# Performance work log

Measured on AMD Instinct MI355X. Metric: run time of the kernel, lower is better.

Reference implementation:

```python
import jax, jax.numpy as jnp
import numpy as np
import math

B, C, H, WIN = 8, 96, 224, 7
D_STATE, DT_RANK = 16, 6
PERK = C // 4
K_RATIO = 0.25


def nearest_perfect_square(val):
    if val <= 0:
        return 0
    s = math.sqrt(val)
    lo = math.floor(s) ** 2
    hi = math.ceil(s) ** 2
    return lo if abs(lo - val) <= abs(hi - val) else hi


def setup_inputs() -> dict:
    key = jax.random.key(0)
    ks = jax.random.split(key, 8)
    x = jax.random.normal(ks[0], (B, C, H, H), dtype=jnp.float32)
    router_w1 = jax.random.normal(ks[1], (C // 4, C), jnp.float32) * (1.0 / math.sqrt(C))
    router_b1 = jnp.zeros((C // 4,), jnp.float32)
    router_w2 = jax.random.normal(ks[2], (1, C // 4), jnp.float32) * (1.0 / math.sqrt(C // 4))
    router_b2 = jnp.zeros((1,), jnp.float32)
    x_proj_weight = jax.random.normal(ks[3], (4, DT_RANK + 2 * D_STATE, PERK), jnp.float32) * (1.0 / math.sqrt(PERK))
    std = DT_RANK ** -0.5
    dt_projs_weight = jax.random.uniform(ks[4], (4, PERK, DT_RANK), jnp.float32, -std, std)
    dt = jnp.exp(jax.random.uniform(ks[5], (4, PERK), jnp.float32) * (math.log(0.1) - math.log(0.001)) + math.log(0.001))
    dt = jnp.clip(dt, 1e-4)
    dt_projs_bias = dt + jnp.log(-jnp.expm1(-dt))  # inv-softplus init as in dt_init_fn
    A_logs = jnp.log(jnp.tile(jnp.arange(1, D_STATE + 1, dtype=jnp.float32)[None, :], (4 * PERK, 1)))
    Ds = jnp.ones((4 * PERK,), jnp.float32)
    return {"x": x, "router_w1": router_w1, "router_b1": router_b1, "router_w2": router_w2,
            "router_b2": router_b2, "x_proj_weight": x_proj_weight, "dt_projs_weight": dt_projs_weight,
            "dt_projs_bias": dt_projs_bias, "A_logs": A_logs, "Ds": Ds}


def reference(x, router_w1, router_b1, router_w2, router_b2, x_proj_weight,
              dt_projs_weight, dt_projs_bias, A_logs, Ds):
    Bb, Cc, Hh, Ww = x.shape
    nH = Hh // WIN
    N = nH * nH
    # window partition: b c (nh p1) (nw p2) -> b (nh nw) c p1 p2
    windows = x.reshape(Bb, Cc, nH, WIN, nH, WIN).transpose(0, 2, 4, 1, 3, 5).reshape(Bb, N, Cc, WIN, WIN)
    # router scores
    pooled = windows.mean(axis=(-2, -1))  # [B,N,C]
    hid = jax.nn.gelu(pooled @ router_w1.T + router_b1, approximate=False)
    logits = (hid @ router_w2.T + router_b2)[..., 0]  # [B,N]
    probs = jax.nn.softmax(logits, axis=1)
    top_k = min(max(nearest_perfect_square(N * K_RATIO), 1), N)
    n = int(math.isqrt(top_k))
    rw, sel = jax.lax.top_k(probs, top_k)  # sorted descending, like torch.topk
    windows_flat = windows.reshape(Bb, N, -1)
    cur = jnp.take_along_axis(windows_flat, sel[:, :, None], axis=1)  # [B,topk,C*w*w]
    cur = cur.reshape(Bb, n, n, Cc, WIN, WIN)
    L = n * n * WIN * WIN
    # channel interleave (p k) -> (k p), k=4
    x_int = cur.reshape(Bb, n, n, Cc // 4, 4, WIN, WIN).transpose(0, 1, 2, 4, 3, 5, 6)  # [B,n,n,4,perK,w,w]

    def local_scan(w, column_first, flip):
        # w: [B,n,n,D,wh,ww] -> [B,D,L]
        if column_first:
            w = w.transpose(0, 3, 2, 1, 5, 4)
        else:
            w = w.transpose(0, 3, 1, 2, 4, 5)
        w = w.reshape(Bb, -1, L)
        if flip:
            w = w[..., ::-1]
        return w

    xs = jnp.stack([
        local_scan(x_int[:, :, :, 0], False, False),
        local_scan(x_int[:, :, :, 1], True, False),
        local_scan(x_int[:, :, :, 2], False, True),
        local_scan(x_int[:, :, :, 3], True, True),
    ], axis=1)  # [B,4,perK,L]

    x_dbl = jnp.einsum('bkdl,kcd->bkcl', xs, x_proj_weight)
    dts = x_dbl[:, :, :DT_RANK]
    Bmat = x_dbl[:, :, DT_RANK:DT_RANK + D_STATE]  # [B,4,Nst,L]
    Cmat = x_dbl[:, :, DT_RANK + D_STATE:]
    dts = jnp.einsum('bkrl,kdr->bkdl', dts, dt_projs_weight)  # [B,4,perK,L]
    A_g = -jnp.exp(A_logs).reshape(4, PERK, D_STATE)
    delta = jax.nn.softplus(dts + dt_projs_bias.reshape(4, PERK)[None, :, :, None])

    # selective scan (grouped): h_{l} = exp(delta*A)*h_{l-1} + delta*u*B_l ; y_l = <h_l, C_l>
    dl = jnp.moveaxis(delta, -1, 0)  # [L,B,4,perK]
    ul = jnp.moveaxis(xs, -1, 0)
    Bl = jnp.moveaxis(Bmat, -1, 0)   # [L,B,4,Nst]
    Cl = jnp.moveaxis(Cmat, -1, 0)
    h0 = jnp.zeros((Bb, 4, PERK, D_STATE), jnp.float32)

    def step(h, inp):
        d, u, Bt, Ct = inp
        h = jnp.exp(d[..., None] * A_g) * h + (d * u)[..., None] * Bt[:, :, None, :]
        return h, jnp.einsum('bkdn,bkn->bkd', h, Ct)

    _, ys = jax.lax.scan(step, h0, (dl, ul, Bl, Cl))
    y = jnp.moveaxis(ys, 0, -1) + xs * Ds.reshape(4, PERK)[None, :, :, None]  # [B,4,perK,L]

    def local_reverse(yk, column_first, flip):
        if flip:
            yk = yk[..., ::-1]
        if column_first:
            yk = yk.reshape(Bb, -1, n, n, WIN, WIN).transpose(0, 1, 3, 5, 2, 4).reshape(Bb, -1, L)
        else:
            yk = yk.reshape(Bb, -1, n, n, WIN, WIN).transpose(0, 1, 2, 4, 3, 5).reshape(Bb, -1, L)
        return yk

    yout = jnp.concatenate([
        local_reverse(y[:, 0], False, False),
        local_reverse(y[:, 1], True, False),
        local_reverse(y[:, 2], False, True),
        local_reverse(y[:, 3], True, True),
    ], axis=1)  # [B,C,L]
    yout = yout.reshape(Bb, Cc, n * n, WIN * WIN).transpose(0, 2, 1, 3).reshape(Bb, top_k, -1)
    cur_out = yout * rw[:, :, None]
    residual = windows_flat * probs[:, :, None]
    residual = residual.at[jnp.arange(Bb)[:, None], sel].set(cur_out)
    new = windows_flat + residual
    return new.reshape(Bb, Cc, -1)
```

## Files before the change

### kernel.cpp

```cpp
#include <hip/hip_runtime.h>
#include <math.h>

#define BBATCH 8
#define CC 96
#define HH 224
#define NHW 32
#define NWIN 1024
#define TOPK 256
#define PERK 24
#define DST 16
#define DTR 6
#define LL 12544
#define LCP 52
#define NG 13
#define TCH 256
#define NBK 32
#define XROW 1248
#define WST4 2080

#define OFF_POOL 0
#define OFF_LOG  786432
#define OFF_PROB 794624
#define OFF_RW   802816
#define OFF_RANK 804864
#define OFF_SEL  813056
#define OFF_WEFF 815104
#define OFF_CP   820480
#define OFF_CS   3966208
#define OFF_XSD  7111936
#define OFF_STG  17335552

#define ROR_ADD(v, CTRL) \
    v += __int_as_float(__builtin_amdgcn_update_dpp(0, __float_as_int(v), CTRL, 0xf, 0xf, true))

__device__ __forceinline__ unsigned f2b(float f) {
    unsigned u = __float_as_uint(f);
    return (u + 0x7fffu + ((u >> 16) & 1u)) >> 16;
}
__device__ __forceinline__ unsigned pk(float a, float b) {
    return f2b(a) | (f2b(b) << 16);
}
__device__ __forceinline__ float lo_f(unsigned w) { return __uint_as_float(w << 16); }
__device__ __forceinline__ float hi_f(unsigned w) { return __uint_as_float(w & 0xffff0000u); }

__global__ void k_pool(const float* __restrict__ x, float* __restrict__ pooled) {
    int bc = blockIdx.x;
    const float* xp = x + (size_t)bc * HH * HH;
    float* pp = pooled + (size_t)bc * NWIN;
    for (int w = threadIdx.x; w < NWIN; w += blockDim.x) {
        int wr = w >> 5, wc = w & 31;
        const float* base = xp + (wr * 7) * HH + wc * 7;
        float s = 0.f;
        #pragma unroll
        for (int i = 0; i < 7; ++i) {
            #pragma unroll
            for (int j = 0; j < 7; ++j) s += base[i * HH + j];
        }
        pp[w] = s * (1.0f / 49.0f);
    }
}

__global__ __launch_bounds__(64) void k_router(
        const float* __restrict__ pooled,
        const float* __restrict__ w1, const float* __restrict__ b1,
        const float* __restrict__ w2, const float* __restrict__ b2,
        const float* __restrict__ xpw, const float* __restrict__ dtw,
        float* __restrict__ wcomb, float* __restrict__ logits) {
    __shared__ float sw1[PERK * CC];
    __shared__ float sb1[PERK];
    __shared__ float sw2[PERK];
    int b = blockIdx.x >> 4, slice = blockIdx.x & 15;
    int tid = threadIdx.x;
    for (int i = blockIdx.x * 64 + tid; i < 4 * 56 * PERK; i += 128 * 64) {
        int k = i / (56 * PERK), rem = i - k * (56 * PERK);
        int row = rem / PERK, c = rem - row * PERK;
        float v;
        if (row < PERK) {
            v = 0.f;
            #pragma unroll
            for (int r = 0; r < DTR; ++r)
                v += dtw[(k * PERK + row) * DTR + r] * xpw[(k * 38 + r) * PERK + c];
        } else {
            v = xpw[(k * 38 + (row - PERK + DTR)) * PERK + c];
        }
        wcomb[i] = v;
    }
    for (int i = tid; i < PERK * CC; i += 64) sw1[i] = w1[i];
    if (tid < PERK) { sb1[tid] = b1[tid]; sw2[tid] = w2[tid]; }
    __syncthreads();
    int w = slice * 64 + tid;
    float hid[PERK];
    #pragma unroll
    for (int j = 0; j < PERK; ++j) hid[j] = sb1[j];
    const float* pp = pooled + (size_t)b * CC * NWIN + w;
    for (int c = 0; c < CC; ++c) {
        float pv = pp[(size_t)c * NWIN];
        #pragma unroll
        for (int j = 0; j < PERK; ++j) hid[j] += pv * sw1[j * CC + c];
    }
    float lg = b2[0];
    #pragma unroll
    for (int j = 0; j < PERK; ++j) {
        float hv = hid[j];
        float g = 0.5f * hv * (1.0f + erff(hv * 0.7071067811865476f));
        lg += g * sw2[j];
    }
    logits[b * NWIN + w] = lg;
}

__global__ __launch_bounds__(64) void k_rankF(const float* __restrict__ logits,
        float* __restrict__ probs, float* __restrict__ rw,
        int* __restrict__ rank, int* __restrict__ sel) {
    __shared__ __attribute__((aligned(16))) float sp[NWIN];
    __shared__ float red[64];
    int b = blockIdx.x >> 4, slice = blockIdx.x & 15;
    int tid = threadIdx.x;
    for (int i = tid; i < NWIN / 4; i += 64)
        ((float4*)sp)[i] = ((const float4*)(logits + (size_t)b * NWIN))[i];
    __syncthreads();
    float m = -1e30f;
    for (int i = tid; i < NWIN; i += 64) m = fmaxf(m, sp[i]);
    red[tid] = m; __syncthreads();
    for (int o = 32; o > 0; o >>= 1) { if (tid < o) red[tid] = fmaxf(red[tid], red[tid + o]); __syncthreads(); }
    float mx = red[0]; __syncthreads();
    for (int i = tid; i < NWIN; i += 64) sp[i] = expf(sp[i] - mx);
    __syncthreads();
    float s = 0.f;
    for (int i = tid; i < NWIN; i += 64) s += sp[i];
    red[tid] = s; __syncthreads();
    for (int o = 32; o > 0; o >>= 1) { if (tid < o) red[tid] += red[tid + o]; __syncthreads(); }
    float sum = red[0]; __syncthreads();
    for (int i = tid; i < NWIN; i += 64) sp[i] = sp[i] / sum;
    __syncthreads();
    int w = slice * 64 + tid;
    float p = sp[w];
    probs[b * NWIN + w] = p;
    int r = 0;
    for (int j = 0; j < NWIN; j += 4) {
        float4 pj = *(const float4*)&sp[j];
        r += (int)((pj.x > p) || (pj.x == p && (j + 0) < w));
        r += (int)((pj.y > p) || (pj.y == p && (j + 1) < w));
        r += (int)((pj.z > p) || (pj.z == p && (j + 2) < w));
        r += (int)((pj.w > p) || (pj.w == p && (j + 3) < w));
    }
    rank[b * NWIN + w] = r;
    if (r < TOPK) { sel[b * TOPK + r] = w; rw[b * TOPK + r] = p; }
}

__device__ __forceinline__ float softplus_f(float v) {
    return fmaxf(v, 0.f) + __logf(1.0f + __expf(-fabsf(v)));
}

__device__ __forceinline__ int window_wsel(const int* sel, int b, int k, int t) {
    int qscan = (k >= 2) ? (255 - t) : t;
    int selidx = (k & 1) ? (((qscan & 15) << 4) | (qscan >> 4)) : qscan;
    return sel[b * TOPK + selidx];
}

__global__ __launch_bounds__(256) void k_gather(const float* __restrict__ x,
        const int* __restrict__ sel, float* __restrict__ xsd) {
    const int total = NBK * TCH * XROW;
    for (int e = blockIdx.x * 256 + threadIdx.x; e < total; e += gridDim.x * 256) {
        int blk = e / XROW;
        int rem = e - blk * XROW;
        int d2 = rem / LCP, j = rem - d2 * LCP;
        float v = 0.f;
        if (j < 49) {
            int t = blk & 255, bk = blk >> 8, k = bk & 3, b = bk >> 2;
            int wsel = window_wsel(sel, b, k, t);
            int pix = (k >= 2) ? 48 - j : j;
            int q7 = pix / 7, r7 = pix - q7 * 7;
            int wi = (k & 1) ? r7 : q7;
            int wj = (k & 1) ? q7 : r7;
            v = x[(((size_t)b * CC + 4 * d2 + k) * HH + (wsel >> 5) * 7 + wi) * HH
                  + (wsel & 31) * 7 + wj];
        }
        xsd[e] = v;
    }
}

__global__ __launch_bounds__(384, 4) void k_prodT(
        const float* __restrict__ xsd, const float* __restrict__ wcomb,
        const float* __restrict__ dtb, const float* __restrict__ alogs,
        float* __restrict__ stage, float* __restrict__ carrP, float* __restrict__ carrS) {
    __shared__ __attribute__((aligned(16))) float sxs[PERK][LCP];
    __shared__ __attribute__((aligned(16))) float sprj[56][LCP];
    __shared__ float swt[56 * PERK];
    __shared__ float sbias[PERK];
    int blk = blockIdx.x; int k = (blk >> 8) & 3;
    int tid = threadIdx.x;
    const float4* xin = (const float4*)(xsd + (size_t)blk * XROW);
    for (int i = tid; i < XROW / 4; i += 384) ((float4*)sxs)[i] = xin[i];
    for (int i = tid; i < 56 * PERK; i += 384) swt[i] = wcomb[k * (56 * PERK) + i];
    if (tid < PERK) sbias[tid] = dtb[k * PERK + tid];
    if (tid < 168) { int r = tid / 3, j = 49 + tid % 3; sprj[r][j] = 0.f; }
    __syncthreads();
    if (tid < 28 * NG) {
        int rp = tid / NG, g = tid - rp * NG; int j = g * 4;
        int row0 = rp * 2, row1 = row0 + 1;
        bool isdl = (row0 < PERK);
        float bs0 = isdl ? sbias[row0] : 0.f;
        float bs1 = isdl ? sbias[row1] : 0.f;
        float a0x = bs0, a0y = bs0, a0z = bs0, a0w = bs0;
        float a1x = bs1, a1y = bs1, a1z = bs1, a1w = bs1;
        #pragma unroll
        for (int d2 = 0; d2 < PERK; ++d2) {
            float w0 = swt[row0 * PERK + d2];
            float w1 = swt[row1 * PERK + d2];
            float4 v = *(const float4*)&sxs[d2][j];
            a0x += w0 * v.x; a0y += w0 * v.y; a0z += w0 * v.z; a0w += w0 * v.w;
            a1x += w1 * v.x; a1y += w1 * v.y; a1z += w1 * v.z; a1w += w1 * v.w;
        }
        if (isdl) {
            a0x = softplus_f(a0x); a0y = softplus_f(a0y); a0z = softplus_f(a0z); a0w = softplus_f(a0w);
            a1x = softplus_f(a1x); a1y = softplus_f(a1y); a1z = softplus_f(a1z); a1w = softplus_f(a1w);
        }
        if (g < 12) {
            float4 o0 = {a0x, a0y, a0z, a0w}; *(float4*)&sprj[row0][j] = o0;
            float4 o1 = {a1x, a1y, a1z, a1w}; *(float4*)&sprj[row1][j] = o1;
        } else {
            sprj[row0][j] = a0x; sprj[row1][j] = a1x;
        }
    }
    __syncthreads();
    uint4* sgP = (uint4*)(stage + (size_t)blk * WST4);
    uint4* sgQ = sgP + 312;
    for (int tsk = tid; tsk < 312; tsk += 384) {
        int g4 = tsk / 24, d2 = tsk - g4 * 24; int j = g4 * 4;
        uint4 o;
        o.x = pk(sprj[d2][j + 0], sxs[d2][j + 0]);
        o.y = pk(sprj[d2][j + 1], sxs[d2][j + 1]);
        o.z = pk(sprj[d2][j + 2], sxs[d2][j + 2]);
        o.w = pk(sprj[d2][j + 3], sxs[d2][j + 3]);
        sgP[tsk] = o;
    }
    for (int tsk = tid; tsk < 208; tsk += 384) {
        int g4 = tsk / 16, s2 = tsk - g4 * 16; int j = g4 * 4;
        uint4 o;
        o.x = pk(sprj[24 + s2][j + 0], sprj[40 + s2][j + 0]);
        o.y = pk(sprj[24 + s2][j + 1], sprj[40 + s2][j + 1]);
        o.z = pk(sprj[24 + s2][j + 2], sprj[40 + s2][j + 2]);
        o.w = pk(sprj[24 + s2][j + 3], sprj[40 + s2][j + 3]);
        sgQ[tsk] = o;
    }
    int d = tid >> 4, s = tid & 15;
    float A = -__expf(alogs[(k * PERK + d) * DST + s]);
    float P = 1.f, S = 0.f;
    for (int g = 0; g < NG; ++g) {
        int j = g * 4;
        float4 dl4 = *(const float4*)&sprj[d][j];
        float4 xs4 = *(const float4*)&sxs[d][j];
        float4 B4  = *(const float4*)&sprj[24 + s][j];
        float aa;
        aa = __expf(dl4.x * A); S = aa * S + (dl4.x * xs4.x) * B4.x; P *= aa;
        aa = __expf(dl4.y * A); S = aa * S + (dl4.y * xs4.y) * B4.y; P *= aa;
        aa = __expf(dl4.z * A); S = aa * S + (dl4.z * xs4.z) * B4.z; P *= aa;
        aa = __expf(dl4.w * A); S = aa * S + (dl4.w * xs4.w) * B4.w; P *= aa;
    }
    size_t cidx = (size_t)blk * 384 + tid;
    carrP[cidx] = P; carrS[cidx] = S;
}

__global__ void k_carry(const float* carrP, const float* carrS, float* hin) {
    int gid = blockIdx.x * blockDim.x + threadIdx.x;
    int bk = gid / 384, ds = gid - bk * 384;
    float Hv = 0.f;
    for (int t = 0; t < TCH; ++t) {
        size_t idx = ((size_t)bk * TCH + t) * 384 + ds;
        float pv = carrP[idx], sv = carrS[idx];
        hin[idx] = Hv;
        Hv = pv * Hv + sv;
    }
}

__global__ __launch_bounds__(64) void k_base(const float* __restrict__ x,
        const float* __restrict__ probs, const int* __restrict__ rank,
        float* __restrict__ out) {
    int wr = blockIdx.x % NHW; int bc = blockIdx.x / NHW;
    int b = bc / CC;
    __shared__ float buf[7 * HH];
    __shared__ float fmul[NHW];
    __shared__ int   fsel[NHW];
    int tid = threadIdx.x;
    const float* xp = x + ((size_t)bc * HH + wr * 7) * HH;
    for (int i = tid; i < 7 * HH; i += 64) buf[i] = xp[i];
    if (tid < NHW) {
        int w = wr * NHW + tid;
        fsel[tid] = (rank[b * NWIN + w] < TOPK);
        fmul[tid] = 1.0f + probs[b * NWIN + w];
    }
    __syncthreads();
    int c = bc - b * CC;
    for (int idx = tid; idx < NHW * 49; idx += 64) {
        int wc = idx / 49, r = idx - wc * 49;
        if (fsel[wc]) continue;
        int ri = r / 7, rj = r - ri * 7;
        float v = buf[ri * HH + wc * 7 + rj];
        int w = wr * NHW + wc;
        out[(((size_t)b * NWIN + w) * CC + c) * 49 + r] = v * fmul[wc];
    }
}

#define BSTEP(pw, qw, jj)                                                          \
    {                                                                              \
        float dl_ = lo_f(pw), xs_ = hi_f(pw), Bv_ = lo_f(qw), Cv_ = hi_f(qw);      \
        float aa_ = __expf(dl_ * A);                                               \
        h = aa_ * h + (dl_ * xs_) * Bv_;                                           \
        float part_ = h * Cv_;                                                     \
        ROR_ADD(part_, 0x121); ROR_ADD(part_, 0x122);                              \
        ROR_ADD(part_, 0x124); ROR_ADD(part_, 0x128);                              \
        if (s == 0 && (jj) < 49) sy[d][jj] = part_ + xs_ * Dsr;                    \
    }

__global__ __launch_bounds__(384, 4) void k_scanT(
        const float* __restrict__ alogs, const float* __restrict__ dsv,
        const float* __restrict__ hin, const float* __restrict__ stage,
        float* __restrict__ xsd) {
    __shared__ __attribute__((aligned(16))) float sy[PERK][LCP];
    int blk = blockIdx.x; int k = (blk >> 8) & 3;
    int tid = threadIdx.x;
    int d = tid >> 4, s = tid & 15;
    float A = -__expf(alogs[(k * PERK + d) * DST + s]);
    float Dsr = dsv[k * PERK + d];
    size_t cidx = (size_t)blk * 384 + tid;
    float h = hin[cidx];
    const uint4* pP = (const uint4*)(stage + (size_t)blk * WST4) + d;
    const uint4* pQ = (const uint4*)(stage + (size_t)blk * WST4) + 312 + s;
    uint4 P0 = pP[0],  Q0 = pQ[0];
    uint4 P1 = pP[24], Q1 = pQ[16];
    uint4 P2 = pP[48], Q2 = pQ[32];
    for (int g4 = 0; g4 < NG; ++g4) {
        uint4 P4 = P0, Q4 = Q0;
        P0 = P1; Q0 = Q1; P1 = P2; Q1 = Q2;
        if (g4 + 3 < NG) { P2 = pP[(g4 + 3) * 24]; Q2 = pQ[(g4 + 3) * 16]; }
        int j = g4 * 4;
        BSTEP(P4.x, Q4.x, j);
        BSTEP(P4.y, Q4.y, j + 1);
        BSTEP(P4.z, Q4.z, j + 2);
        BSTEP(P4.w, Q4.w, j + 3);
    }
    __syncthreads();
    float* yout = xsd + (size_t)blk * XROW;
    for (int idx = tid; idx < PERK * 49; idx += 384) {
        int j = idx / PERK, d2 = idx - j * PERK;
        yout[idx] = sy[d2][j];
    }
}

__global__ __launch_bounds__(256) void k_yadd(const float* __restrict__ ysrc,
        const float* __restrict__ x, const int* __restrict__ sel,
        const float* __restrict__ rw, float* __restrict__ out) {
    __shared__ float ytile[CC * 49];
    int qo = blockIdx.x & 255; int b = blockIdx.x >> 8;
    int wsel = sel[b * TOPK + qo];
    float p = rw[b * TOPK + qo];
    for (int idx = threadIdx.x; idx < CC * 49; idx += 256) {
        int k = idx / 1176; int r1 = idx - k * 1176;
        int u = r1 / 168;   int r2 = r1 - u * 168;
        int wj = r2 / 24;   int d = r2 - wj * 24;
        int rest = qo * 7 + u;
        int b2 = rest & 15; int aw = rest >> 4;
        int wi = aw % 7;    int a = aw / 7;
        int q   = (k & 1) ? (b2 * 16 + a) : (a * 16 + b2);
        int pix = (k & 1) ? (wj * 7 + wi) : (wi * 7 + wj);
        int uu = q * 49 + pix;
        int l = (k >= 2) ? (LL - 1 - uu) : uu;
        int bk = b * 4 + k;
        int t2 = l / 49, jj = l - t2 * 49;
        ytile[(k * PERK + d) * 49 + u * 7 + wj] =
            p * ysrc[((size_t)(bk * 256 + t2)) * XROW + jj * PERK + d];
    }
    __syncthreads();
    float* ob = out + ((size_t)(b * NWIN + wsel) * CC) * 49;
    int gi0 = (wsel >> 5) * 7, gj0 = (wsel & 31) * 7;
    for (int e = threadIdx.x; e < CC * 49; e += 256) {
        int C = e / 49, cell = e - C * 49;
        int u = cell / 7, wj = cell - u * 7;
        float xv = x[(((size_t)b * CC + C) * HH + gi0 + u) * HH + gj0 + wj];
        ob[e] = xv + ytile[e];
    }
}

extern "C" void kernel_launch(void* const* d_in, const int* in_sizes, int n_in,
                              void* d_out, int out_size, void* d_ws, size_t ws_size,
                              hipStream_t stream) {
    const float* x   = (const float*)d_in[0];
    const float* w1  = (const float*)d_in[1];
    const float* b1  = (const float*)d_in[2];
    const float* w2  = (const float*)d_in[3];
    const float* b2  = (const float*)d_in[4];
    const float* xpw = (const float*)d_in[5];
    const float* dtw = (const float*)d_in[6];
    const float* dtb = (const float*)d_in[7];
    const float* alg = (const float*)d_in[8];
    const float* dsv = (const float*)d_in[9];
    float* out = (float*)d_out;
    float* ws  = (float*)d_ws;

    float* pooled = ws + OFF_POOL;
    float* logits = ws + OFF_LOG;
    float* probs  = ws + OFF_PROB;
    float* rwv    = ws + OFF_RW;
    int*   rank   = (int*)(ws + OFF_RANK);
    int*   sel    = (int*)(ws + OFF_SEL);
    float* wcomb  = ws + OFF_WEFF;
    float* cP  = ws + OFF_CP;
    float* cS  = ws + OFF_CS;
    float* xsd = ws + OFF_XSD;
    float* stage = ws + OFF_STG;

    k_pool  <<<BBATCH * CC, 256, 0, stream>>>(x, pooled);
    k_router<<<BBATCH * 16, 64, 0, stream>>>(pooled, w1, b1, w2, b2, xpw, dtw, wcomb, logits);
    k_rankF <<<BBATCH * 16, 64, 0, stream>>>(logits, probs, rwv, rank, sel);
    k_gather<<<2048, 256, 0, stream>>>(x, sel, xsd);
    k_prodT <<<NBK * TCH, 384, 0, stream>>>(xsd, wcomb, dtb, alg, stage, cP, cS);
    k_carry <<<48, 256, 0, stream>>>(cP, cS, cP);
    k_base  <<<BBATCH * CC * NHW, 64, 0, stream>>>(x, probs, rank, out);
    k_scanT <<<NBK * TCH, 384, 0, stream>>>(alg, dsv, cP, stage, xsd);
    k_yadd  <<<BBATCH * TOPK, 256, 0, stream>>>(xsd, x, sel, rwv, out);
}
```

Baseline: 433.3 us.

## Fuse carry and base kernels, scan two chunks per block, use exp2

The carry-propagation kernel and the non-selected-window base kernel are merged into one launch, with the first 48 blocks running the carry recurrence and the remaining blocks (now 256 threads) doing the base copy. The chunk scan kernel now handles two independent chunks per block, interleaving their recurrences to expose more instruction-level parallelism behind the serial exp/DPP chain, with prefetch depth cut from 3 to 2. Exponentials switch to exp2f with A pre-scaled by log2(e). The cost is higher register pressure in the scan and a mixed-role fused kernel whose slow carry blocks may straggle.

After: 463.2 us. +6.9%, slower.

```diff
diff --git a/kernel.cpp b/kernel.cpp
--- a/kernel.cpp
+++ b/kernel.cpp
@@ -17,6 +17,7 @@
 #define NBK 32
 #define XROW 1248
 #define WST4 2080
+#define LOG2E 1.4426950408889634f
 
 #define OFF_POOL 0
 #define OFF_LOG  786432
@@ -244,7 +245,7 @@
         sgQ[tsk] = o;
     }
     int d = tid >> 4, s = tid & 15;
-    float A = -__expf(alogs[(k * PERK + d) * DST + s]);
+    float A2 = -__expf(alogs[(k * PERK + d) * DST + s]) * LOG2E;
     float P = 1.f, S = 0.f;
     for (int g = 0; g < NG; ++g) {
         int j = g * 4;
@@ -252,38 +253,39 @@
         float4 xs4 = *(const float4*)&sxs[d][j];
         float4 B4  = *(const float4*)&sprj[24 + s][j];
         float aa;
-        aa = __expf(dl4.x * A); S = aa * S + (dl4.x * xs4.x) * B4.x; P *= aa;
-        aa = __expf(dl4.y * A); S = aa * S + (dl4.y * xs4.y) * B4.y; P *= aa;
-        aa = __expf(dl4.z * A); S = aa * S + (dl4.z * xs4.z) * B4.z; P *= aa;
-        aa = __expf(dl4.w * A); S = aa * S + (dl4.w * xs4.w) * B4.w; P *= aa;
+        aa = exp2f(dl4.x * A2); S = aa * S + (dl4.x * xs4.x) * B4.x; P *= aa;
+        aa = exp2f(dl4.y * A2); S = aa * S + (dl4.y * xs4.y) * B4.y; P *= aa;
+        aa = exp2f(dl4.z * A2); S = aa * S + (dl4.z * xs4.z) * B4.z; P *= aa;
+        aa = exp2f(dl4.w * A2); S = aa * S + (dl4.w * xs4.w) * B4.w; P *= aa;
     }
     size_t cidx = (size_t)blk * 384 + tid;
     carrP[cidx] = P; carrS[cidx] = S;
 }
 
-__global__ void k_carry(const float* carrP, const float* carrS, float* hin) {
-    int gid = blockIdx.x * blockDim.x + threadIdx.x;
-    int bk = gid / 384, ds = gid - bk * 384;
-    float Hv = 0.f;
-    for (int t = 0; t < TCH; ++t) {
-        size_t idx = ((size_t)bk * TCH + t) * 384 + ds;
-        float pv = carrP[idx], sv = carrS[idx];
-        hin[idx] = Hv;
-        Hv = pv * Hv + sv;
-    }
-}
-
-__global__ __launch_bounds__(64) void k_base(const float* __restrict__ x,
-        const float* __restrict__ probs, const int* __restrict__ rank,
-        float* __restrict__ out) {
-    int wr = blockIdx.x % NHW; int bc = blockIdx.x / NHW;
+__global__ __launch_bounds__(256) void k_cb(const float* carrP, const float* carrS,
+        float* hin, const float* __restrict__ x, const float* __restrict__ probs,
+        const int* __restrict__ rank, float* __restrict__ out) {
+    if (blockIdx.x < 48) {
+        int gid = blockIdx.x * 256 + threadIdx.x;
+        int bk = gid / 384, ds = gid - bk * 384;
+        float Hv = 0.f;
+        for (int t = 0; t < TCH; ++t) {
+            size_t idx = ((size_t)bk * TCH + t) * 384 + ds;
+            float pv = carrP[idx], sv = carrS[idx];
+            hin[idx] = Hv;
+            Hv = pv * Hv + sv;
+        }
+        return;
+    }
+    int bid = blockIdx.x - 48;
+    int wr = bid % NHW; int bc = bid / NHW;
     int b = bc / CC;
     __shared__ float buf[7 * HH];
     __shared__ float fmul[NHW];
     __shared__ int   fsel[NHW];
     int tid = threadIdx.x;
     const float* xp = x + ((size_t)bc * HH + wr * 7) * HH;
-    for (int i = tid; i < 7 * HH; i += 64) buf[i] = xp[i];
+    for (int i = tid; i < 7 * HH; i += 256) buf[i] = xp[i];
     if (tid < NHW) {
         int w = wr * NHW + tid;
         fsel[tid] = (rank[b * NWIN + w] < TOPK);
@@ -291,7 +293,7 @@
     }
     __syncthreads();
     int c = bc - b * CC;
-    for (int idx = tid; idx < NHW * 49; idx += 64) {
+    for (int idx = tid; idx < NHW * 49; idx += 256) {
         int wc = idx / 49, r = idx - wc * 49;
         if (fsel[wc]) continue;
         int ri = r / 7, rj = r - ri * 7;
@@ -301,49 +303,57 @@
     }
 }
 
-#define BSTEP(pw, qw, jj)                                                          \
+#define BST(hv, widx, pw, qw, jj)                                                  \
     {                                                                              \
         float dl_ = lo_f(pw), xs_ = hi_f(pw), Bv_ = lo_f(qw), Cv_ = hi_f(qw);      \
-        float aa_ = __expf(dl_ * A);                                               \
-        h = aa_ * h + (dl_ * xs_) * Bv_;                                           \
-        float part_ = h * Cv_;                                                     \
+        float aa_ = exp2f(dl_ * A2);                                               \
+        hv = aa_ * hv + (dl_ * xs_) * Bv_;                                         \
+        float part_ = hv * Cv_;                                                    \
         ROR_ADD(part_, 0x121); ROR_ADD(part_, 0x122);                              \
         ROR_ADD(part_, 0x124); ROR_ADD(part_, 0x128);                              \
-        if (s == 0 && (jj) < 49) sy[d][jj] = part_ + xs_ * Dsr;                    \
+        if (s == 0 && (jj) < 49) sy[widx][d][jj] = part_ + xs_ * Dsr;              \
     }
 
 __global__ __launch_bounds__(384, 4) void k_scanT(
         const float* __restrict__ alogs, const float* __restrict__ dsv,
         const float* __restrict__ hin, const float* __restrict__ stage,
         float* __restrict__ xsd) {
-    __shared__ __attribute__((aligned(16))) float sy[PERK][LCP];
-    int blk = blockIdx.x; int k = (blk >> 8) & 3;
+    __shared__ __attribute__((aligned(16))) float sy[2][PERK][LCP];
+    int blk2 = blockIdx.x;
+    int w0 = blk2 * 2, w1 = w0 + 1;
+    int k = (w0 >> 8) & 3;
     int tid = threadIdx.x;
     int d = tid >> 4, s = tid & 15;
-    float A = -__expf(alogs[(k * PERK + d) * DST + s]);
+    float A2 = -__expf(alogs[(k * PERK + d) * DST + s]) * LOG2E;
     float Dsr = dsv[k * PERK + d];
-    size_t cidx = (size_t)blk * 384 + tid;
-    float h = hin[cidx];
-    const uint4* pP = (const uint4*)(stage + (size_t)blk * WST4) + d;
-    const uint4* pQ = (const uint4*)(stage + (size_t)blk * WST4) + 312 + s;
-    uint4 P0 = pP[0],  Q0 = pQ[0];
-    uint4 P1 = pP[24], Q1 = pQ[16];
-    uint4 P2 = pP[48], Q2 = pQ[32];
+    float h0 = hin[(size_t)w0 * 384 + tid];
+    float h1 = hin[(size_t)w1 * 384 + tid];
+    const uint4* pP0 = (const uint4*)(stage + (size_t)w0 * WST4) + d;
+    const uint4* pQ0 = (const uint4*)(stage + (size_t)w0 * WST4) + 312 + s;
+    const uint4* pP1 = (const uint4*)(stage + (size_t)w1 * WST4) + d;
+    const uint4* pQ1 = (const uint4*)(stage + (size_t)w1 * WST4) + 312 + s;
+    uint4 P0c = pP0[0],  Q0c = pQ0[0],  P1c = pP1[0],  Q1c = pQ1[0];
+    uint4 P0n = pP0[24], Q0n = pQ0[16], P1n = pP1[24], Q1n = pQ1[16];
     for (int g4 = 0; g4 < NG; ++g4) {
-        uint4 P4 = P0, Q4 = Q0;
-        P0 = P1; Q0 = Q1; P1 = P2; Q1 = Q2;
-        if (g4 + 3 < NG) { P2 = pP[(g4 + 3) * 24]; Q2 = pQ[(g4 + 3) * 16]; }
+        uint4 a0 = P0c, b0 = Q0c, a1 = P1c, b1 = Q1c;
+        P0c = P0n; Q0c = Q0n; P1c = P1n; Q1c = Q1n;
+        if (g4 + 2 < NG) {
+            int jP = (g4 + 2) * 24, jQ = (g4 + 2) * 16;
+            P0n = pP0[jP]; Q0n = pQ0[jQ]; P1n = pP1[jP]; Q1n = pQ1[jQ];
+        }
         int j = g4 * 4;
-        BSTEP(P4.x, Q4.x, j);
-        BSTEP(P4.y, Q4.y, j + 1);
-        BSTEP(P4.z, Q4.z, j + 2);
-        BSTEP(P4.w, Q4.w, j + 3);
-    }
-    __syncthreads();
-    float* yout = xsd + (size_t)blk * XROW;
+        BST(h0, 0, a0.x, b0.x, j);     BST(h1, 1, a1.x, b1.x, j);
+        BST(h0, 0, a0.y, b0.y, j + 1); BST(h1, 1, a1.y, b1.y, j + 1);
+        BST(h0, 0, a0.z, b0.z, j + 2); BST(h1, 1, a1.z, b1.z, j + 2);
+        BST(h0, 0, a0.w, b0.w, j + 3); BST(h1, 1, a1.w, b1.w, j + 3);
+    }
+    __syncthreads();
+    float* y0 = xsd + (size_t)w0 * XROW;
+    float* y1 = xsd + (size_t)w1 * XROW;
     for (int idx = tid; idx < PERK * 49; idx += 384) {
         int j = idx / PERK, d2 = idx - j * PERK;
-        yout[idx] = sy[d2][j];
+        y0[idx] = sy[0][d2][j];
+        y1[idx] = sy[1][d2][j];
     }
 }
 
@@ -414,8 +424,7 @@
     k_rankF <<<BBATCH * 16, 64, 0, stream>>>(logits, probs, rwv, rank, sel);
     k_gather<<<2048, 256, 0, stream>>>(x, sel, xsd);
     k_prodT <<<NBK * TCH, 384, 0, stream>>>(xsd, wcomb, dtb, alg, stage, cP, cS);
-    k_carry <<<48, 256, 0, stream>>>(cP, cS, cP);
-    k_base  <<<BBATCH * CC * NHW, 64, 0, stream>>>(x, probs, rank, out);
-    k_scanT <<<NBK * TCH, 384, 0, stream>>>(alg, dsv, cP, stage, xsd);
+    k_cb    <<<48 + BBATCH * CC * NHW, 256, 0, stream>>>(cP, cS, cP, x, probs, rank, out);
+    k_scanT <<<NBK * TCH / 2, 384, 0, stream>>>(alg, dsv, cP, stage, xsd);
     k_yadd  <<<BBATCH * TOPK, 256, 0, stream>>>(xsd, x, sel, rwv, out);
 }
```
